# Kernel optimization log

Hardware: AMD Instinct MI355X
Metric: run time of the kernel (lower is better)

Reference implementation:

```python
import jax, jax.numpy as jnp
import numpy as np

N_HEADS = 16
HEAD_DIM = 128
ROPE_BASE = 10000.0


def _apply_rope(x, start_pos):
    # x: [B, T, H, Dh]; interleaved-pair RoPE (llama-style)
    B, T, H, Dh = x.shape
    half = Dh // 2
    inv_freq = 1.0 / (ROPE_BASE ** (jnp.arange(0, Dh, 2, dtype=jnp.float32) / Dh))  # [half]
    pos = jnp.arange(T, dtype=jnp.float32) + start_pos                              # [T]
    ang = pos[:, None] * inv_freq[None, :]                                          # [T, half]
    cos = jnp.cos(ang)[None, :, None, :].astype(x.dtype)                            # [1,T,1,half]
    sin = jnp.sin(ang)[None, :, None, :].astype(x.dtype)
    x1 = x[..., 0::2]
    x2 = x[..., 1::2]
    r1 = x1 * cos - x2 * sin
    r2 = x1 * sin + x2 * cos
    return jnp.stack([r1, r2], axis=-1).reshape(B, T, H, Dh)


def setup_inputs() -> dict:
    key = jax.random.key(0)
    k0, k1, k2, k3, k4 = jax.random.split(key, 5)
    B, T, D = 2, 2048, 2048
    d_lat = 1024
    x = jax.random.normal(k0, (B, T, D), dtype=jnp.float32)
    wq = jax.random.normal(k1, (D, N_HEADS * HEAD_DIM), dtype=jnp.float32) / np.sqrt(D)
    w_down = jax.random.normal(k2, (D, d_lat), dtype=jnp.float32) / np.sqrt(D)
    w_up = jax.random.normal(k3, (d_lat, 2 * N_HEADS * HEAD_DIM), dtype=jnp.float32) / np.sqrt(d_lat)
    wo = jax.random.normal(k4, (N_HEADS * HEAD_DIM, D), dtype=jnp.float32) / np.sqrt(N_HEADS * HEAD_DIM)
    return {"x": x, "wq": wq, "w_down": w_down, "w_up": w_up, "wo": wo}


def reference(x, wq, w_down, w_up, wo):
    # Prefill path: use_cache=False, mask=None -> causal, start_pos=0, n_kv_heads==n_heads
    B, T, D = x.shape
    H, Dh = N_HEADS, HEAD_DIM
    scale = Dh ** -0.5

    q = (x @ wq).reshape(B, T, H, Dh)
    c_kv = x @ w_down                               # [B, T, d_latent]
    kv_up = (c_kv @ w_up).reshape(B, T, H, 2 * Dh)  # latent decompression
    k, v = kv_up[..., :Dh], kv_up[..., Dh:]

    q = _apply_rope(q, 0)
    k = _apply_rope(k, 0)

    scores = jnp.einsum('bqhd,bkhd->bhqk', q, k) * scale  # [B,H,T,T]
    causal = jnp.tril(jnp.ones((T, T), dtype=bool))
    scores = jnp.where(causal[None, None, :, :], scores, jnp.float32(-jnp.inf))
    attn = jax.nn.softmax(scores, axis=-1)
    out = jnp.einsum('bhqk,bkhd->bqhd', attn, v).reshape(B, T, H * Dh)
    return out @ wo
```

## Files before the change

kernel.cpp:

```cpp
#include <hip/hip_runtime.h>
#include <math.h>
#include <stdint.h>

#define T_SEQ 2048
#define DMODEL 2048
#define DLAT 1024
#define NH 16
#define DH 128
#define BATCH 2
#define MTOT (BATCH * T_SEQ)

typedef float f32x4 __attribute__((ext_vector_type(4)));
typedef __bf16 bf16x8 __attribute__((ext_vector_type(8)));

__device__ __forceinline__ unsigned short f2bf(float f) {
    union { float f; unsigned u; } v; v.f = f;
    unsigned r = (v.u + 0x7fffu + ((v.u >> 16) & 1u)) >> 16;
    return (unsigned short)r;
}

#define GLL16(g, l) __builtin_amdgcn_global_load_lds( \
    (const __attribute__((address_space(1))) unsigned int*)(g), \
    (__attribute__((address_space(3))) unsigned int*)(l), 16, 0, 0)

__global__ void rope_table_kernel(float* __restrict__ cosb, float* __restrict__ sinb) {
    int idx = blockIdx.x * blockDim.x + threadIdx.x;
    if (idx >= T_SEQ * 64) return;
    int t = idx >> 6;
    int i = idx & 63;
    float inv = expf(-((2.0f * (float)i) / 128.0f) * logf(10000.0f));
    float ang = (float)t * inv;
    cosb[idx] = cosf(ang);
    sinb[idx] = sinf(ang);
}

__global__ void conv_f2b_kernel(const float* __restrict__ s, unsigned short* __restrict__ d) {
    int i = (blockIdx.x * blockDim.x + threadIdx.x) * 4;
    float4 v = *(const float4*)(s + i);
    ushort4 o;
    o.x = f2bf(v.x); o.y = f2bf(v.y); o.z = f2bf(v.z); o.w = f2bf(v.w);
    *(ushort4*)(d + i) = o;
}

__global__ void transpose_f2b_kernel(const float* __restrict__ src, unsigned short* __restrict__ dst,
                                     int R, int C) {
    __shared__ unsigned short tile[32][33];
    int tx = threadIdx.x & 31, ty = threadIdx.x >> 5;
    int r0 = blockIdx.y * 32, c0 = blockIdx.x * 32;
#pragma unroll
    for (int i = 0; i < 32; i += 8)
        tile[ty + i][tx] = f2bf(src[(size_t)(r0 + ty + i) * C + c0 + tx]);
    __syncthreads();
#pragma unroll
    for (int i = 0; i < 32; i += 8)
        dst[(size_t)(c0 + ty + i) * R + r0 + tx] = tile[tx][ty + i];
}

__global__ void transpose_b2b_kernel(const unsigned short* __restrict__ src, unsigned short* __restrict__ dst,
                                     int R, int C) {
    __shared__ unsigned short tile[32][33];
    int tx = threadIdx.x & 31, ty = threadIdx.x >> 5;
    int r0 = blockIdx.y * 32, c0 = blockIdx.x * 32;
#pragma unroll
    for (int i = 0; i < 32; i += 8)
        tile[ty + i][tx] = src[(size_t)(r0 + ty + i) * C + c0 + tx];
    __syncthreads();
#pragma unroll
    for (int i = 0; i < 32; i += 8)
        dst[(size_t)(c0 + ty + i) * R + r0 + tx] = tile[tx][ty + i];
}

template <int EPI>
__global__ __launch_bounds__(256)
void gemm_bf16_kernel(const unsigned short* __restrict__ A, const unsigned short* __restrict__ BT,
                      void* __restrict__ C0, void* __restrict__ C1,
                      const float* __restrict__ cosb, const float* __restrict__ sinb,
                      int M, int N, int K) {
    __shared__ unsigned short As[128 * 32];
    __shared__ unsigned short Bs[128 * 32];
    const int t = threadIdx.x;
    const int w = t >> 6, l = t & 63;
    const int wr = w >> 1, wc = w & 1;
    const int lr = l & 15, lg = l >> 4;
    const int m0 = blockIdx.y * 128, n0 = blockIdx.x * 128;

    f32x4 acc[4][4] = {{}};

    const unsigned short* aP  = A  + (size_t)(m0 + (t >> 2)) * K + (t & 3) * 8;
    const unsigned short* aP2 = aP + (size_t)64 * K;
    const unsigned short* bP  = BT + (size_t)(n0 + (t >> 2)) * K + (t & 3) * 8;
    const unsigned short* bP2 = bP + (size_t)64 * K;

    for (int k0 = 0; k0 < K; k0 += 32) {
        __syncthreads();
        GLL16(aP  + k0, &As[t * 8]);
        GLL16(aP2 + k0, &As[2048 + t * 8]);
        GLL16(bP  + k0, &Bs[t * 8]);
        GLL16(bP2 + k0, &Bs[2048 + t * 8]);
        __syncthreads();

        bf16x8 af[4], bfr[4];
#pragma unroll
        for (int i = 0; i < 4; ++i)
            af[i] = *(const bf16x8*)&As[(wr * 64 + i * 16 + lr) * 32 + lg * 8];
#pragma unroll
        for (int j = 0; j < 4; ++j)
            bfr[j] = *(const bf16x8*)&Bs[(wc * 64 + j * 16 + lr) * 32 + lg * 8];
#pragma unroll
        for (int i = 0; i < 4; ++i)
#pragma unroll
            for (int j = 0; j < 4; ++j)
                acc[i][j] = __builtin_amdgcn_mfma_f32_16x16x32_bf16(af[i], bfr[j], acc[i][j], 0, 0, 0);
    }

    const bool is_v = (EPI == 2) && ((n0 & 128) != 0);
#pragma unroll
    for (int i = 0; i < 4; ++i) {
#pragma unroll
        for (int j = 0; j < 4; ++j) {
#pragma unroll
            for (int rr = 0; rr < 4; ++rr) {
                const int row_g = m0 + wr * 64 + i * 16 + lg * 4 + rr;
                const int col_g = n0 + wc * 64 + j * 16 + lr;
                float v = acc[i][j][rr];
                if (EPI == 0) {
                    ((unsigned short*)C0)[(size_t)row_g * N + col_g] = f2bf(v);
                } else if (EPI == 1) {
                    float o_ = __shfl_xor(v, 1);
                    int d = col_g & 127;
                    int tp = row_g & (T_SEQ - 1);
                    float c = cosb[tp * 64 + (d >> 1)];
                    float s = sinb[tp * 64 + (d >> 1)];
                    float res = (lr & 1) ? (o_ * s + v * c) : (v * c - o_ * s);
                    ((unsigned short*)C0)[(size_t)row_g * N + col_g] = f2bf(res);
                } else if (EPI == 2) {
                    float res = v;
                    if (!is_v) {
                        float o_ = __shfl_xor(v, 1);
                        int d = col_g & 127;
                        int tp = row_g & (T_SEQ - 1);
                        float c = cosb[tp * 64 + (d >> 1)];
                        float s = sinb[tp * 64 + (d >> 1)];
                        res = (lr & 1) ? (o_ * s + v * c) : (v * c - o_ * s);
                    }
                    int dcol = ((col_g >> 8) << 7) | (col_g & 127);
                    unsigned short* dst = is_v ? (unsigned short*)C1 : (unsigned short*)C0;
                    dst[(size_t)row_g * DMODEL + dcol] = f2bf(res);
                } else {
                    ((float*)C0)[(size_t)row_g * N + col_g] = v;
                }
            }
        }
    }
}

__global__ __launch_bounds__(256, 2)
void attn_mfma2_kernel(const unsigned short* __restrict__ qb, const unsigned short* __restrict__ kb,
                       const unsigned short* __restrict__ vT, unsigned short* __restrict__ ob) {
    __shared__ __align__(16) unsigned short Ks[2][64 * 128];
    __shared__ __align__(16) unsigned short Vs[128 * 64];
    __shared__ __align__(16) unsigned short Ps[4][16][64];

    const int bh = blockIdx.x;
    const int b = bh >> 4, h = bh & 15;
    const int qt = 15 - blockIdx.y;
    const int t = threadIdx.x;
    const int w = t >> 6, l = t & 63;
    const int lr = l & 15, lg = l >> 4;

    const unsigned short* kbase = kb + (size_t)(b * T_SEQ) * DMODEL + h * DH;
    const unsigned short* vbase = vT + (size_t)(h * DH) * MTOT + (size_t)b * T_SEQ;
    const float sc = 0.08838834764831845f;

    const int q0 = qt * 128;
    const int q_base = q0 + w * 32;

    bf16x8 qf[2][4];
#pragma unroll
    for (int rg = 0; rg < 2; ++rg) {
        const unsigned short* qrow = qb + (size_t)(b * T_SEQ + q_base + rg * 16 + lr) * DMODEL + h * DH;
#pragma unroll
        for (int c = 0; c < 4; ++c) qf[rg][c] = *(const bf16x8*)(qrow + c * 32 + lg * 8);
    }

    f32x4 o[2][8] = {{}};
    float m[2][4], lsum[2][4];
#pragma unroll
    for (int rg = 0; rg < 2; ++rg)
#pragma unroll
        for (int r = 0; r < 4; ++r) { m[rg][r] = -3.0e38f; lsum[rg][r] = 0.f; }

    const int nt = 2 * qt + 2;
    int cur = 0;

#pragma unroll
    for (int i = 0; i < 4; ++i) {
        int c = i * 256 + t;
        int row = c >> 4;
        int k16 = (c & 15) ^ (row & 7);
        GLL16(kbase + (size_t)row * DMODEL + k16 * 8, &Ks[0][c * 8]);
    }
    __syncthreads();

    for (int kt = 0; kt < nt; ++kt) {
        const int k0 = kt * 64;
        if (kt + 1 < nt) {
            const int kn = k0 + 64;
#pragma unroll
            for (int i = 0; i < 4; ++i) {
                int c = i * 256 + t;
                int row = c >> 4;
                int k16 = (c & 15) ^ (row & 7);
                GLL16(kbase + (size_t)(kn + row) * DMODEL + k16 * 8, &Ks[cur ^ 1][c * 8]);
            }
        }
#pragma unroll
        for (int i = 0; i < 4; ++i) {
            int c = i * 256 + t;
            int d = c >> 3;
            int k8 = (c & 7) ^ (d & 7);
            GLL16(vbase + (size_t)d * MTOT + k0 + k8 * 8, &Vs[c * 8]);
        }

        f32x4 s[2][4] = {{}};
#pragma unroll
        for (int j = 0; j < 4; ++j) {
            const int krow = j * 16 + lr;
#pragma unroll
            for (int c = 0; c < 4; ++c) {
                bf16x8 kf = *(const bf16x8*)&Ks[cur][krow * 128 + (((c * 4 + lg) ^ (krow & 7)) * 8)];
                s[0][j] = __builtin_amdgcn_mfma_f32_16x16x32_bf16(qf[0][c], kf, s[0][j], 0, 0, 0);
                s[1][j] = __builtin_amdgcn_mfma_f32_16x16x32_bf16(qf[1][c], kf, s[1][j], 0, 0, 0);
            }
        }

        float al[2][4];
#pragma unroll
        for (int rg = 0; rg < 2; ++rg) {
            const int qb0 = q_base + rg * 16;
#pragma unroll
            for (int j = 0; j < 4; ++j)
#pragma unroll
                for (int r = 0; r < 4; ++r) s[rg][j][r] *= sc;
            if (k0 + 63 > qb0) {
#pragma unroll
                for (int j = 0; j < 4; ++j) {
                    const int key = k0 + j * 16 + lr;
#pragma unroll
                    for (int r = 0; r < 4; ++r)
                        if (key > qb0 + lg * 4 + r) s[rg][j][r] = -3.0e38f;
                }
            }
#pragma unroll
            for (int r = 0; r < 4; ++r) {
                float tm = fmaxf(fmaxf(s[rg][0][r], s[rg][1][r]), fmaxf(s[rg][2][r], s[rg][3][r]));
                tm = fmaxf(tm, __shfl_xor(tm, 1));
                tm = fmaxf(tm, __shfl_xor(tm, 2));
                tm = fmaxf(tm, __shfl_xor(tm, 4));
                tm = fmaxf(tm, __shfl_xor(tm, 8));
                const float mn = fmaxf(m[rg][r], tm);
                const float a = __expf(m[rg][r] - mn);
                m[rg][r] = mn;
                float rs = 0.f;
#pragma unroll
                for (int j = 0; j < 4; ++j) { s[rg][j][r] = __expf(s[rg][j][r] - mn); rs += s[rg][j][r]; }
                rs += __shfl_xor(rs, 1); rs += __shfl_xor(rs, 2);
                rs += __shfl_xor(rs, 4); rs += __shfl_xor(rs, 8);
                lsum[rg][r] = lsum[rg][r] * a + rs;
                al[rg][r] = a;
            }
#pragma unroll
            for (int i = 0; i < 8; ++i)
#pragma unroll
                for (int r = 0; r < 4; ++r) o[rg][i][r] *= al[rg][r];
        }

        __syncthreads();

        bf16x8 pa[2][2];
#pragma unroll
        for (int rg = 0; rg < 2; ++rg) {
#pragma unroll
            for (int j = 0; j < 4; ++j) {
#pragma unroll
                for (int r = 0; r < 4; ++r) {
                    const int prow = lg * 4 + r;
                    const int chunk = (j * 2 + (lr >> 3)) ^ (prow & 7);
                    Ps[w][prow][chunk * 8 + (lr & 7)] = f2bf(s[rg][j][r]);
                }
            }
#pragma unroll
            for (int kc = 0; kc < 2; ++kc)
                pa[rg][kc] = *(const bf16x8*)&Ps[w][lr][((kc * 4 + lg) ^ (lr & 7)) * 8];
        }

#pragma unroll
        for (int i = 0; i < 8; ++i) {
            const int d = i * 16 + lr;
#pragma unroll
            for (int kc = 0; kc < 2; ++kc) {
                bf16x8 vf = *(const bf16x8*)&Vs[d * 64 + (((kc * 4 + lg) ^ (d & 7)) * 8)];
                o[0][i] = __builtin_amdgcn_mfma_f32_16x16x32_bf16(pa[0][kc], vf, o[0][i], 0, 0, 0);
                o[1][i] = __builtin_amdgcn_mfma_f32_16x16x32_bf16(pa[1][kc], vf, o[1][i], 0, 0, 0);
            }
        }
        __syncthreads();
        cur ^= 1;
    }

#pragma unroll
    for (int rg = 0; rg < 2; ++rg) {
        float inv[4];
#pragma unroll
        for (int r = 0; r < 4; ++r) inv[r] = 1.f / lsum[rg][r];
#pragma unroll
        for (int i = 0; i < 8; ++i)
#pragma unroll
            for (int r = 0; r < 4; ++r)
                ob[(size_t)(b * T_SEQ + q_base + rg * 16 + lg * 4 + r) * DMODEL + h * DH + i * 16 + lr]
                    = f2bf(o[rg][i][r] * inv[r]);
    }
}

extern "C" void kernel_launch(void* const* d_in, const int* in_sizes, int n_in,
                              void* d_out, int out_size, void* d_ws, size_t ws_size,
                              hipStream_t stream) {
    const float* x      = (const float*)d_in[0];
    const float* wq     = (const float*)d_in[1];
    const float* w_down = (const float*)d_in[2];
    const float* w_up   = (const float*)d_in[3];
    const float* wo     = (const float*)d_in[4];
    float* out = (float*)d_out;

    uint8_t* p = (uint8_t*)d_ws;
    float* cosb = (float*)p;            p += (size_t)T_SEQ * 64 * 4;
    float* sinb = (float*)p;            p += (size_t)T_SEQ * 64 * 4;
    unsigned short* xb   = (unsigned short*)p; p += (size_t)MTOT * DMODEL * 2;
    unsigned short* wqT  = (unsigned short*)p; p += (size_t)DMODEL * DMODEL * 2;
    unsigned short* wdT  = (unsigned short*)p; p += (size_t)DLAT * DMODEL * 2;
    unsigned short* wuT  = (unsigned short*)p; p += (size_t)(2 * NH * DH) * DLAT * 2;
    unsigned short* woT  = (unsigned short*)p; p += (size_t)DMODEL * DMODEL * 2;
    unsigned short* qbuf = (unsigned short*)p; p += (size_t)MTOT * DMODEL * 2;
    unsigned short* ckv  = (unsigned short*)p; p += (size_t)MTOT * DLAT * 2;
    unsigned short* kbuf = (unsigned short*)p; p += (size_t)MTOT * DMODEL * 2;
    unsigned short* vbuf = (unsigned short*)p; p += (size_t)MTOT * DMODEL * 2;
    unsigned short* vT   = (unsigned short*)p; p += (size_t)DMODEL * MTOT * 2;
    unsigned short* abuf = xb;

    rope_table_kernel<<<(T_SEQ * 64) / 256, 256, 0, stream>>>(cosb, sinb);
    conv_f2b_kernel<<<(MTOT * DMODEL / 4) / 256, 256, 0, stream>>>(x, xb);
    transpose_f2b_kernel<<<dim3(DMODEL / 32, DMODEL / 32), 256, 0, stream>>>(wq, wqT, DMODEL, DMODEL);
    transpose_f2b_kernel<<<dim3(DLAT / 32, DMODEL / 32), 256, 0, stream>>>(w_down, wdT, DMODEL, DLAT);
    transpose_f2b_kernel<<<dim3((2 * NH * DH) / 32, DLAT / 32), 256, 0, stream>>>(w_up, wuT, DLAT, 2 * NH * DH);
    transpose_f2b_kernel<<<dim3(DMODEL / 32, DMODEL / 32), 256, 0, stream>>>(wo, woT, DMODEL, DMODEL);

    gemm_bf16_kernel<1><<<dim3(DMODEL / 128, MTOT / 128), 256, 0, stream>>>(
        xb, wqT, qbuf, nullptr, cosb, sinb, MTOT, DMODEL, DMODEL);
    gemm_bf16_kernel<0><<<dim3(DLAT / 128, MTOT / 128), 256, 0, stream>>>(
        xb, wdT, ckv, nullptr, cosb, sinb, MTOT, DLAT, DMODEL);
    gemm_bf16_kernel<2><<<dim3((2 * NH * DH) / 128, MTOT / 128), 256, 0, stream>>>(
        ckv, wuT, kbuf, vbuf, cosb, sinb, MTOT, 2 * NH * DH, DLAT);
    transpose_b2b_kernel<<<dim3(DMODEL / 32, MTOT / 32), 256, 0, stream>>>(vbuf, vT, MTOT, DMODEL);
    attn_mfma2_kernel<<<dim3(BATCH * NH, 16), 256, 0, stream>>>(qbuf, kbuf, vT, abuf);
    gemm_bf16_kernel<3><<<dim3(DMODEL / 128, MTOT / 128), 256, 0, stream>>>(
        abuf, woT, out, nullptr, cosb, sinb, MTOT, DMODEL, DMODEL);
}
```

Before: 508.3 us.

## Fuse Q and latent-down GEMMs; streamline attention softmax with lazy rescale

Merges the Q projection (with RoPE) and the latent down-projection into one GEMM launch. This relies on wqT and wdT sitting next to each other in memory, so the N dimension simply extends to 3072 and the epilogue routes columns by n0. In attention, the softmax moves to base-2 exponentials with the scale pre-multiplied by log2(e). Row max and row sum now use DPP reductions instead of shuffles, and the running-max rescale of the output accumulators is skipped unless some row's max grows by more than 8 (in log2 units). MFMA sections are wrapped in s_setprio, and float-to-bf16 conversion uses the native cast. These changes target launch overhead, exp and reduction instruction count, and redundant rescale multiplies. The trade-off is that un-rescaled exponentials can reach up to 2^8 before the bf16 P conversion.

```diff
diff --git a/kernel.cpp b/kernel.cpp
--- a/kernel.cpp
+++ b/kernel.cpp
@@ -14,9 +14,32 @@
 typedef __bf16 bf16x8 __attribute__((ext_vector_type(8)));
 
 __device__ __forceinline__ unsigned short f2bf(float f) {
-    union { float f; unsigned u; } v; v.f = f;
-    unsigned r = (v.u + 0x7fffu + ((v.u >> 16) & 1u)) >> 16;
-    return (unsigned short)r;
+    return __builtin_bit_cast(unsigned short, (__bf16)f);
+}
+
+#define EXP2F(x) __builtin_amdgcn_exp2f(x)
+
+__device__ __forceinline__ float red16_max(float v) {
+    int x = __builtin_bit_cast(int, v);
+    v = fmaxf(v, __builtin_bit_cast(float, __builtin_amdgcn_update_dpp(x, x, 0xB1, 0xf, 0xf, false)));
+    x = __builtin_bit_cast(int, v);
+    v = fmaxf(v, __builtin_bit_cast(float, __builtin_amdgcn_update_dpp(x, x, 0x4E, 0xf, 0xf, false)));
+    x = __builtin_bit_cast(int, v);
+    v = fmaxf(v, __builtin_bit_cast(float, __builtin_amdgcn_update_dpp(x, x, 0x124, 0xf, 0xf, false)));
+    x = __builtin_bit_cast(int, v);
+    v = fmaxf(v, __builtin_bit_cast(float, __builtin_amdgcn_update_dpp(x, x, 0x128, 0xf, 0xf, false)));
+    return v;
+}
+__device__ __forceinline__ float red16_sum(float v) {
+    int x = __builtin_bit_cast(int, v);
+    v += __builtin_bit_cast(float, __builtin_amdgcn_update_dpp(x, x, 0xB1, 0xf, 0xf, false));
+    x = __builtin_bit_cast(int, v);
+    v += __builtin_bit_cast(float, __builtin_amdgcn_update_dpp(x, x, 0x4E, 0xf, 0xf, false));
+    x = __builtin_bit_cast(int, v);
+    v += __builtin_bit_cast(float, __builtin_amdgcn_update_dpp(x, x, 0x124, 0xf, 0xf, false));
+    x = __builtin_bit_cast(int, v);
+    v += __builtin_bit_cast(float, __builtin_amdgcn_update_dpp(x, x, 0x128, 0xf, 0xf, false));
+    return v;
 }
 
 #define GLL16(g, l) __builtin_amdgcn_global_load_lds( \
@@ -113,7 +136,8 @@
                 acc[i][j] = __builtin_amdgcn_mfma_f32_16x16x32_bf16(af[i], bfr[j], acc[i][j], 0, 0, 0);
     }
 
-    const bool is_v = (EPI == 2) && ((n0 & 128) != 0);
+    const bool is_v  = (EPI == 2) && ((n0 & 128) != 0);
+    const bool is_cv = (EPI == 4) && (n0 >= 2048);
 #pragma unroll
     for (int i = 0; i < 4; ++i) {
 #pragma unroll
@@ -123,17 +147,7 @@
                 const int row_g = m0 + wr * 64 + i * 16 + lg * 4 + rr;
                 const int col_g = n0 + wc * 64 + j * 16 + lr;
                 float v = acc[i][j][rr];
-                if (EPI == 0) {
-                    ((unsigned short*)C0)[(size_t)row_g * N + col_g] = f2bf(v);
-                } else if (EPI == 1) {
-                    float o_ = __shfl_xor(v, 1);
-                    int d = col_g & 127;
-                    int tp = row_g & (T_SEQ - 1);
-                    float c = cosb[tp * 64 + (d >> 1)];
-                    float s = sinb[tp * 64 + (d >> 1)];
-                    float res = (lr & 1) ? (o_ * s + v * c) : (v * c - o_ * s);
-                    ((unsigned short*)C0)[(size_t)row_g * N + col_g] = f2bf(res);
-                } else if (EPI == 2) {
+                if (EPI == 2) {
                     float res = v;
                     if (!is_v) {
                         float o_ = __shfl_xor(v, 1);
@@ -146,8 +160,20 @@
                     int dcol = ((col_g >> 8) << 7) | (col_g & 127);
                     unsigned short* dst = is_v ? (unsigned short*)C1 : (unsigned short*)C0;
                     dst[(size_t)row_g * DMODEL + dcol] = f2bf(res);
+                } else if (EPI == 3) {
+                    ((float*)C0)[(size_t)row_g * N + col_g] = v;
                 } else {
-                    ((float*)C0)[(size_t)row_g * N + col_g] = v;
+                    if (!is_cv) {
+                        float o_ = __shfl_xor(v, 1);
+                        int d = col_g & 127;
+                        int tp = row_g & (T_SEQ - 1);
+                        float c = cosb[tp * 64 + (d >> 1)];
+                        float s = sinb[tp * 64 + (d >> 1)];
+                        float res = (lr & 1) ? (o_ * s + v * c) : (v * c - o_ * s);
+                        ((unsigned short*)C0)[(size_t)row_g * DMODEL + col_g] = f2bf(res);
+                    } else {
+                        ((unsigned short*)C1)[(size_t)row_g * DLAT + (col_g - 2048)] = f2bf(v);
+                    }
                 }
             }
         }
@@ -170,7 +196,7 @@
 
     const unsigned short* kbase = kb + (size_t)(b * T_SEQ) * DMODEL + h * DH;
     const unsigned short* vbase = vT + (size_t)(h * DH) * MTOT + (size_t)b * T_SEQ;
-    const float sc = 0.08838834764831845f;
+    const float sc2 = 0.08838834764831845f * 1.44269504089f;
 
     const int q0 = qt * 128;
     const int q_base = q0 + w * 32;
@@ -223,6 +249,7 @@
         }
 
         f32x4 s[2][4] = {{}};
+        __builtin_amdgcn_s_setprio(1);
 #pragma unroll
         for (int j = 0; j < 4; ++j) {
             const int krow = j * 16 + lr;
@@ -233,15 +260,15 @@
                 s[1][j] = __builtin_amdgcn_mfma_f32_16x16x32_bf16(qf[1][c], kf, s[1][j], 0, 0, 0);
             }
         }
-
-        float al[2][4];
+        __builtin_amdgcn_s_setprio(0);
+
 #pragma unroll
         for (int rg = 0; rg < 2; ++rg) {
             const int qb0 = q_base + rg * 16;
 #pragma unroll
             for (int j = 0; j < 4; ++j)
 #pragma unroll
-                for (int r = 0; r < 4; ++r) s[rg][j][r] *= sc;
+                for (int r = 0; r < 4; ++r) s[rg][j][r] *= sc2;
             if (k0 + 63 > qb0) {
 #pragma unroll
                 for (int j = 0; j < 4; ++j) {
@@ -251,28 +278,32 @@
                         if (key > qb0 + lg * 4 + r) s[rg][j][r] = -3.0e38f;
                 }
             }
+            float tm[4];
+            int need = 0;
 #pragma unroll
             for (int r = 0; r < 4; ++r) {
-                float tm = fmaxf(fmaxf(s[rg][0][r], s[rg][1][r]), fmaxf(s[rg][2][r], s[rg][3][r]));
-                tm = fmaxf(tm, __shfl_xor(tm, 1));
-                tm = fmaxf(tm, __shfl_xor(tm, 2));
-                tm = fmaxf(tm, __shfl_xor(tm, 4));
-                tm = fmaxf(tm, __shfl_xor(tm, 8));
-                const float mn = fmaxf(m[rg][r], tm);
-                const float a = __expf(m[rg][r] - mn);
-                m[rg][r] = mn;
+                float v = fmaxf(fmaxf(s[rg][0][r], s[rg][1][r]), fmaxf(s[rg][2][r], s[rg][3][r]));
+                tm[r] = red16_max(v);
+                need |= (tm[r] - m[rg][r] > 8.0f) ? 1 : 0;
+            }
+            if (__any(need)) {
+#pragma unroll
+                for (int r = 0; r < 4; ++r) {
+                    const float mn = fmaxf(m[rg][r], tm[r]);
+                    const float a = EXP2F(m[rg][r] - mn);
+                    m[rg][r] = mn;
+                    lsum[rg][r] *= a;
+#pragma unroll
+                    for (int i = 0; i < 8; ++i) o[rg][i][r] *= a;
+                }
+            }
+#pragma unroll
+            for (int r = 0; r < 4; ++r) {
                 float rs = 0.f;
 #pragma unroll
-                for (int j = 0; j < 4; ++j) { s[rg][j][r] = __expf(s[rg][j][r] - mn); rs += s[rg][j][r]; }
-                rs += __shfl_xor(rs, 1); rs += __shfl_xor(rs, 2);
-                rs += __shfl_xor(rs, 4); rs += __shfl_xor(rs, 8);
-                lsum[rg][r] = lsum[rg][r] * a + rs;
-                al[rg][r] = a;
-            }
-#pragma unroll
-            for (int i = 0; i < 8; ++i)
-#pragma unroll
-                for (int r = 0; r < 4; ++r) o[rg][i][r] *= al[rg][r];
+                for (int j = 0; j < 4; ++j) { s[rg][j][r] = EXP2F(s[rg][j][r] - m[rg][r]); rs += s[rg][j][r]; }
+                lsum[rg][r] += red16_sum(rs);
+            }
         }
 
         __syncthreads();
@@ -294,6 +325,7 @@
                 pa[rg][kc] = *(const bf16x8*)&Ps[w][lr][((kc * 4 + lg) ^ (lr & 7)) * 8];
         }
 
+        __builtin_amdgcn_s_setprio(1);
 #pragma unroll
         for (int i = 0; i < 8; ++i) {
             const int d = i * 16 + lr;
@@ -304,6 +336,7 @@
                 o[1][i] = __builtin_amdgcn_mfma_f32_16x16x32_bf16(pa[1][kc], vf, o[1][i], 0, 0, 0);
             }
         }
+        __builtin_amdgcn_s_setprio(0);
         __syncthreads();
         cur ^= 1;
     }
@@ -354,10 +387,8 @@
     transpose_f2b_kernel<<<dim3((2 * NH * DH) / 32, DLAT / 32), 256, 0, stream>>>(w_up, wuT, DLAT, 2 * NH * DH);
     transpose_f2b_kernel<<<dim3(DMODEL / 32, DMODEL / 32), 256, 0, stream>>>(wo, woT, DMODEL, DMODEL);
 
-    gemm_bf16_kernel<1><<<dim3(DMODEL / 128, MTOT / 128), 256, 0, stream>>>(
-        xb, wqT, qbuf, nullptr, cosb, sinb, MTOT, DMODEL, DMODEL);
-    gemm_bf16_kernel<0><<<dim3(DLAT / 128, MTOT / 128), 256, 0, stream>>>(
-        xb, wdT, ckv, nullptr, cosb, sinb, MTOT, DLAT, DMODEL);
+    gemm_bf16_kernel<4><<<dim3((DMODEL + DLAT) / 128, MTOT / 128), 256, 0, stream>>>(
+        xb, wqT, qbuf, ckv, cosb, sinb, MTOT, DMODEL + DLAT, DMODEL);
     gemm_bf16_kernel<2><<<dim3((2 * NH * DH) / 128, MTOT / 128), 256, 0, stream>>>(
         ckv, wuT, kbuf, vbuf, cosb, sinb, MTOT, 2 * NH * DH, DLAT);
     transpose_b2b_kernel<<<dim3(DMODEL / 32, MTOT / 32), 256, 0, stream>>>(vbuf, vT, MTOT, DMODEL);
```

Result: faster. 451.9 us (-11.1%).
